# Kernel tuning notes

Measured on AMD Instinct MI355X. Metric: run time of the kernel, lower is better.

The kernel has to match this reference:

```python
import jax, jax.numpy as jnp
import numpy as np

E = 8          # num_experts
K = 2          # top-k experts per token
CAP_RATIO = 1.05


def setup_inputs() -> dict:
    key = jax.random.key(0)
    k0, k1, k2, k3 = jax.random.split(key, 4)
    B, S, D, H = 2, 2048, 512, 2048
    return {
        "x": jax.random.normal(k0, (B, S, D), jnp.float32),
        "gate_w": jax.random.normal(k1, (E, D), jnp.float32) * (1.0 / np.sqrt(D)),
        "fc1_w": jax.random.normal(k2, (E, D, H), jnp.float32) * (1.0 / np.sqrt(D)),
        "fc1_b": jnp.zeros((E, H), jnp.float32),
        "fc2_w": jax.random.normal(k3, (E, H, D), jnp.float32) * (1.0 / np.sqrt(H)),
        "fc2_b": jnp.zeros((E, D), jnp.float32),
    }


def reference(x, gate_w, fc1_w, fc1_b, fc2_w, fc2_b):
    B, S, D = x.shape
    xf = x.reshape(-1, D)               # [T, D]
    T = xf.shape[0]

    # ---- router (eval mode: no noise) ----
    logits = xf @ gate_w.T              # [T, E]
    gates = jax.nn.softmax(logits, axis=-1)
    top_g, top_i = jax.lax.top_k(gates, K)   # [T, K]

    # importance auxiliary loss (std unbiased=False == jnp.std default)
    imp = gates.sum(axis=0)                  # [E]
    imp_loss = (jnp.std(imp) / (imp.mean() + 1e-6)) ** 2

    # ---- capacity-limited dispatch mask ----
    # torch loops slot-major: slot 0 over all tokens in order, then slot 1.
    # position of each (slot, token) entry within its expert's queue:
    buffer_cap = round(K * T * CAP_RATIO / E)
    idx_sm = top_i.T.reshape(-1)                        # [K*T] slot-major
    oh = jax.nn.one_hot(idx_sm, E, dtype=jnp.int32)     # [K*T, E]
    pos = jnp.cumsum(oh, axis=0) - oh                   # earlier same-expert count
    pos_e = jnp.take_along_axis(pos, idx_sm[:, None], axis=1)[:, 0]
    within = (pos_e < buffer_cap).reshape(K, T).T       # [T, K] bool

    wf = within.astype(xf.dtype)
    oh_tke = jax.nn.one_hot(top_i, E, dtype=xf.dtype) * wf[..., None]  # dispatch mask [T,K,E]
    combine_te = jnp.einsum('tk,tke->te', top_g * wf, oh_tke / jnp.maximum(oh_tke, 1e-30) * oh_tke) if False else jnp.einsum('tk,tke->te', top_g * wf, jax.nn.one_hot(top_i, E, dtype=xf.dtype))

    # load-balance loss from post-capacity token counts
    tokens_per_expert = oh_tke.sum(axis=(0, 1))         # [E]
    l_load = (jnp.std(tokens_per_expert) / (tokens_per_expert.mean() + 1e-6)) ** 2
    l_aux = 0.5 * (imp_loss + l_load)

    # ---- per-expert MLP (dense compute, masked combine) ----
    h = jnp.einsum('td,edh->teh', xf, fc1_w) + fc1_b[None]      # [T, E, H]
    h = jax.nn.gelu(h, approximate=False)                       # torch nn.GELU default
    y = jnp.einsum('teh,ehd->ted', h, fc2_w) + fc2_b[None]      # [T, E, D]

    out = jnp.einsum('te,ted->td', combine_te, y).reshape(B, S, D)
    return out, l_aux, l_load
```

## Files before the change

### kernel.cpp

```cpp
#include <hip/hip_runtime.h>
#include <hip/hip_bf16.h>

#define E_    8
#define TT    4096
#define DD    512
#define HH    2048
#define CAP   1075
#define MPAD  1152
#define MT    9
#define MT2   18

typedef __bf16 bf16_t;
typedef bf16_t bf16x4 __attribute__((ext_vector_type(4)));
typedef bf16_t bf16x8 __attribute__((ext_vector_type(8)));
typedef float  f32x4  __attribute__((ext_vector_type(4)));
typedef unsigned int u32;

__device__ __forceinline__ bf16_t tobf(float f) { return (bf16_t)f; }

__device__ __forceinline__ float gelu_f(float v) {
  const float u = v * (0.7978845608028654f + 0.035677408136300125f * v * v);
  const float a = __builtin_fabsf(u);
  const float ex = __expf(2.0f * a);
  float th = 1.0f - 2.0f / (ex + 1.0f);
  th = __builtin_copysignf(th, u);
  return 0.5f * v * (1.0f + th);
}

#define OFF_TOPI  256u
#define OFF_TOPG  (OFF_TOPI + 4096u*2u*4u)
#define OFF_SLOT  (OFF_TOPG + 4096u*2u*4u)
#define OFF_ETOK  (OFF_SLOT + 4096u*2u*4u)
#define OFF_XB    (OFF_ETOK + 8u*1152u*4u)
#define XB_BYTES  (4096u*512u*2u)
#define OFF_W1T   (OFF_XB + XB_BYTES)
#define W1T_BYTES (8u*512u*2048u*2u)
#define OFF_W2T   (OFF_W1T + W1T_BYTES)
#define W2T_BYTES (8u*2048u*512u*2u)
#define OFF_H     (OFF_W2T + W2T_BYTES)
#define H_BYTES   (8u*1152u*2048u*2u)
#define OFF_Y     OFF_W1T

__global__ __launch_bounds__(256) void router_kernel(
    const float* __restrict__ x, const float* __restrict__ gw,
    float* __restrict__ imp, int* __restrict__ top_i, float* __restrict__ top_g,
    bf16_t* __restrict__ xb) {
  const int tid = threadIdx.x;
  const int wid = tid >> 6, lane = tid & 63;
  const int t = blockIdx.x * 4 + wid;

  float p[E_];
#pragma unroll
  for (int e = 0; e < E_; ++e) p[e] = 0.f;
  const float* xr = x + (size_t)t * DD;
  bf16_t* xo = xb + (size_t)t * DD;
#pragma unroll
  for (int it = 0; it < 2; ++it) {
    const int d = it * 256 + lane * 4;
    const float4 xv = *(const float4*)(xr + d);
    bf16_t o4[4] = {tobf(xv.x), tobf(xv.y), tobf(xv.z), tobf(xv.w)};
    *(bf16x4*)(xo + d) = *(const bf16x4*)o4;
#pragma unroll
    for (int e = 0; e < E_; ++e) {
      const float4 gv = *(const float4*)(gw + e * DD + d);
      p[e] += xv.x * gv.x + xv.y * gv.y + xv.z * gv.z + xv.w * gv.w;
    }
  }
#pragma unroll
  for (int off = 32; off > 0; off >>= 1) {
#pragma unroll
    for (int e = 0; e < E_; ++e) p[e] += __shfl_down(p[e], off);
  }

  __shared__ float simp[4][E_];
  if (lane == 0) {
    float mx = p[0];
#pragma unroll
    for (int e = 1; e < E_; ++e) mx = fmaxf(mx, p[e]);
    float g[E_]; float s = 0.f;
#pragma unroll
    for (int e = 0; e < E_; ++e) { g[e] = expf(p[e] - mx); s += g[e]; }
    const float inv = 1.f / s;
#pragma unroll
    for (int e = 0; e < E_; ++e) { g[e] *= inv; simp[wid][e] = g[e]; }
    int i0 = 0;
#pragma unroll
    for (int e = 1; e < E_; ++e) if (g[e] > g[i0]) i0 = e;
    int i1 = (i0 == 0) ? 1 : 0;
#pragma unroll
    for (int e = 0; e < E_; ++e) if (e != i0 && g[e] > g[i1]) i1 = e;
    top_i[t * 2 + 0] = i0;  top_i[t * 2 + 1] = i1;
    top_g[t * 2 + 0] = g[i0]; top_g[t * 2 + 1] = g[i1];
  }
  __syncthreads();
  if (tid < E_) {
    const float s = simp[0][tid] + simp[1][tid] + simp[2][tid] + simp[3][tid];
    atomicAdd(&imp[tid], s);
  }
}

__global__ __launch_bounds__(1024) void capacity_kernel(
    const int* __restrict__ top_i, const float* __restrict__ top_g,
    const float* __restrict__ imp, int* __restrict__ etok,
    int* __restrict__ slot_map, int* __restrict__ kept, float* __restrict__ scal) {
  __shared__ u32 wt[16][4];
  const int tid = threadIdx.x, wave = tid >> 6, lane = tid & 63;

  int eidx[8];
#pragma unroll
  for (int q = 0; q < 8; ++q) {
    const int j = tid * 8 + q;
    const int k = j >> 12, t = j & (TT - 1);
    eidx[q] = top_i[t * 2 + k];
  }
  u32 pk[4] = {0u, 0u, 0u, 0u};
#pragma unroll
  for (int q = 0; q < 8; ++q) pk[eidx[q] >> 1] += 1u << ((eidx[q] & 1) * 16);

  u32 v[4] = {pk[0], pk[1], pk[2], pk[3]};
#pragma unroll
  for (int off = 1; off < 64; off <<= 1) {
#pragma unroll
    for (int p = 0; p < 4; ++p) {
      const u32 n = (u32)__shfl_up((int)v[p], off);
      if (lane >= off) v[p] += n;
    }
  }
  if (lane == 63) {
#pragma unroll
    for (int p = 0; p < 4; ++p) wt[wave][p] = v[p];
  }
  __syncthreads();
  u32 base[4] = {0u, 0u, 0u, 0u}, tot[4] = {0u, 0u, 0u, 0u};
#pragma unroll
  for (int w = 0; w < 16; ++w) {
#pragma unroll
    for (int p = 0; p < 4; ++p) {
      const u32 xv = wt[w][p];
      if (w < wave) base[p] += xv;
      tot[p] += xv;
    }
  }
  int run[E_];
#pragma unroll
  for (int p = 0; p < 4; ++p) {
    const u32 excl = base[p] + v[p] - pk[p];
    run[2 * p]     = (int)(excl & 0xFFFFu);
    run[2 * p + 1] = (int)(excl >> 16);
  }
#pragma unroll
  for (int q = 0; q < 8; ++q) {
    const int e = eidx[q];
    const int pos = run[e]++;
    const int j = tid * 8 + q;
    if (pos < CAP) {
      const int k = j >> 12, t = j & (TT - 1);
      etok[e * MPAD + pos] = t;
      slot_map[j] = (e << 16) | pos;
    } else {
      slot_map[j] = -1;
    }
  }
  if (tid == 0) {
    float tpe[E_];
#pragma unroll
    for (int p = 0; p < 4; ++p) {
      const int t0 = (int)(tot[p] & 0xFFFFu), t1 = (int)(tot[p] >> 16);
      const int k0 = t0 < CAP ? t0 : CAP, k1 = t1 < CAP ? t1 : CAP;
      kept[2 * p] = k0; kept[2 * p + 1] = k1;
      tpe[2 * p] = (float)k0; tpe[2 * p + 1] = (float)k1;
    }
    float ms = 0.f;
#pragma unroll
    for (int e = 0; e < E_; ++e) ms += tpe[e];
    ms *= (1.f / E_);
    float vt = 0.f;
#pragma unroll
    for (int e = 0; e < E_; ++e) { const float d = tpe[e] - ms; vt += d * d; }
    vt *= (1.f / E_);
    const float ll = vt / ((ms + 1e-6f) * (ms + 1e-6f));

    float iv[E_], mi = 0.f;
#pragma unroll
    for (int e = 0; e < E_; ++e) { iv[e] = imp[e]; mi += iv[e]; }
    mi *= (1.f / E_);
    float vi = 0.f;
#pragma unroll
    for (int e = 0; e < E_; ++e) { const float d = iv[e] - mi; vi += d * d; }
    vi *= (1.f / E_);
    const float il = vi / ((mi + 1e-6f) * (mi + 1e-6f));

    scal[0] = 0.5f * (il + ll);
    scal[1] = ll;
  }
}

__global__ __launch_bounds__(256) void transpose_both_kernel(
    const float* __restrict__ fc1, bf16_t* __restrict__ w1t,
    const float* __restrict__ fc2, bf16_t* __restrict__ w2t) {
  __shared__ float tile[64][65];
  const int z = blockIdx.z;
  const bool first = (z < 8);
  const int e = first ? z : z - 8;
  const int R = first ? DD : HH;
  const int C = first ? HH : DD;
  const int ct = first ? blockIdx.x : blockIdx.y;
  const int rt = first ? blockIdx.y : blockIdx.x;
  const float* ip = (first ? fc1 : fc2) + (size_t)e * DD * HH;
  bf16_t* op = (first ? w1t : w2t) + (size_t)e * DD * HH;
  const int r0 = rt * 64, c0 = ct * 64;
  const int tid = threadIdx.x;
  const int rr = tid >> 4, c4 = (tid & 15) * 4;
#pragma unroll
  for (int p = 0; p < 4; ++p) {
    const int r = p * 16 + rr;
    const float4 v = *(const float4*)(ip + (size_t)(r0 + r) * C + c0 + c4);
    tile[r][c4 + 0] = v.x; tile[r][c4 + 1] = v.y;
    tile[r][c4 + 2] = v.z; tile[r][c4 + 3] = v.w;
  }
  __syncthreads();
  const int g = tid & 7, ob = tid >> 3;
#pragma unroll
  for (int p = 0; p < 2; ++p) {
    const int oc = p * 32 + ob;
    bf16_t o8[8];
#pragma unroll
    for (int k = 0; k < 8; ++k) o8[k] = tobf(tile[g * 8 + k][oc]);
    *(bf16x8*)(op + (size_t)(c0 + oc) * R + r0 + g * 8) = *(const bf16x8*)o8;
  }
}

template <int MI, int KLEN, int KSTR, bool GATHER>
__device__ __forceinline__ void gemm_core(
    const bf16_t* __restrict__ Abase, const int* __restrict__ rows,
    const bf16_t* __restrict__ B,
    bf16_t* As, bf16_t* Bs, f32x4 (&acc)[4][MI]) {
  const int tid = threadIdx.x;
  const int wave = tid >> 6, lane = tid & 63;
  const int r8 = lane >> 3;
  const int kswz = ((lane & 7) ^ r8) * 8;
  const bf16_t* ga[MI];
#pragma unroll
  for (int p = 0; p < MI; ++p) {
    const int r = wave * (MI * 8) + p * 8 + r8;
    const int trow = GATHER ? rows[r] : r;
    ga[p] = Abase + (size_t)trow * KSTR + kswz;
  }
  const bf16_t* gb = B + (size_t)(wave * 32 + r8) * KSTR + kswz;
  const int mw = (wave >> 1) * (MI * 16), nw = (wave & 1) * 64;
  const int l15 = lane & 15, quad = lane >> 4;
  const int sw = l15 & 7;

  for (int k0 = 0; k0 < KLEN; k0 += 64) {
    __syncthreads();
#pragma unroll
    for (int p = 0; p < MI; ++p) {
      __builtin_amdgcn_global_load_lds(
          (const __attribute__((address_space(1))) void*)(ga[p] + k0),
          (__attribute__((address_space(3))) void*)(As + (wave * (MI * 8) + p * 8) * 64),
          16, 0, 0);
    }
#pragma unroll
    for (int p = 0; p < 4; ++p) {
      __builtin_amdgcn_global_load_lds(
          (const __attribute__((address_space(1))) void*)(gb + (size_t)p * 8 * KSTR + k0),
          (__attribute__((address_space(3))) void*)(Bs + (wave * 32 + p * 8) * 64),
          16, 0, 0);
    }
    __syncthreads();
#pragma unroll
    for (int ks = 0; ks < 2; ++ks) {
      bf16x8 af[MI], bfr[4];
#pragma unroll
      for (int i = 0; i < MI; ++i)
        af[i] = *(const bf16x8*)(As + (mw + i * 16 + l15) * 64 + (((ks * 4 + quad) ^ sw) << 3));
#pragma unroll
      for (int j = 0; j < 4; ++j)
        bfr[j] = *(const bf16x8*)(Bs + (nw + j * 16 + l15) * 64 + (((ks * 4 + quad) ^ sw) << 3));
#pragma unroll
      for (int j = 0; j < 4; ++j)
#pragma unroll
        for (int i = 0; i < MI; ++i)
          acc[j][i] = __builtin_amdgcn_mfma_f32_16x16x32_bf16(bfr[j], af[i], acc[j][i], 0, 0, 0);
    }
  }
}

__global__ __launch_bounds__(256, 4) void gemm1_kernel(
    const bf16_t* __restrict__ xb, const int* __restrict__ etok,
    const int* __restrict__ kept, const bf16_t* __restrict__ W1t,
    const float* __restrict__ b1, bf16_t* __restrict__ Hbuf) {
  const int e = blockIdx.x, tileN = blockIdx.y, tileM = blockIdx.z;
  if (tileM * 128 >= kept[e]) return;
  __shared__ __align__(16) bf16_t As[128 * 64];
  __shared__ __align__(16) bf16_t Bs[128 * 64];
  const bf16_t* B = W1t + ((size_t)e * HH + tileN * 128) * DD;
  f32x4 acc[4][4];
  const f32x4 z = {0.f, 0.f, 0.f, 0.f};
#pragma unroll
  for (int j = 0; j < 4; ++j)
#pragma unroll
    for (int i = 0; i < 4; ++i) acc[j][i] = z;
  gemm_core<4, DD, DD, true>(xb, etok + e * MPAD + tileM * 128, B, As, Bs, acc);

  const int tid = threadIdx.x, wave = tid >> 6, lane = tid & 63;
  const int mw = (wave >> 1) * 64, nw = (wave & 1) * 64;
  const int l15 = lane & 15, quad = lane >> 4;
#pragma unroll
  for (int j = 0; j < 4; ++j) {
    const int n0 = tileN * 128 + nw + j * 16 + quad * 4;
    const float4 b4 = *(const float4*)(b1 + e * HH + n0);
#pragma unroll
    for (int i = 0; i < 4; ++i) {
      const int m = tileM * 128 + mw + i * 16 + l15;
      bf16x4 h4;
      h4.x = tobf(gelu_f(acc[j][i][0] + b4.x));
      h4.y = tobf(gelu_f(acc[j][i][1] + b4.y));
      h4.z = tobf(gelu_f(acc[j][i][2] + b4.z));
      h4.w = tobf(gelu_f(acc[j][i][3] + b4.w));
      *(bf16x4*)(Hbuf + ((size_t)e * MPAD + m) * HH + n0) = h4;
    }
  }
}

__global__ __launch_bounds__(256, 6) void gemm2_kernel(
    const bf16_t* __restrict__ Hbuf, const bf16_t* __restrict__ W2t,
    const int* __restrict__ kept, bf16_t* __restrict__ Ybuf) {
  const int e = blockIdx.x, tileN = blockIdx.y, tileM = blockIdx.z;
  const int nk = kept[e];
  if (tileM * 64 >= nk) return;
  __shared__ __align__(16) bf16_t As[64 * 64];
  __shared__ __align__(16) bf16_t Bs[128 * 64];
  const bf16_t* A = Hbuf + ((size_t)e * MPAD + tileM * 64) * HH;
  const bf16_t* B = W2t + ((size_t)e * DD + tileN * 128) * HH;
  f32x4 acc[4][2];
  const f32x4 z = {0.f, 0.f, 0.f, 0.f};
#pragma unroll
  for (int j = 0; j < 4; ++j)
#pragma unroll
    for (int i = 0; i < 2; ++i) acc[j][i] = z;
  gemm_core<2, HH, HH, false>(A, nullptr, B, As, Bs, acc);

  const int tid = threadIdx.x, wave = tid >> 6, lane = tid & 63;
  const int mw = (wave >> 1) * 32, nw = (wave & 1) * 64;
  const int l15 = lane & 15, quad = lane >> 4;
#pragma unroll
  for (int j = 0; j < 4; ++j) {
    const int n0 = tileN * 128 + nw + j * 16 + quad * 4;
#pragma unroll
    for (int i = 0; i < 2; ++i) {
      const int m = tileM * 64 + mw + i * 16 + l15;
      if (m < nk) {
        bf16x4 o4;
        o4.x = tobf(acc[j][i][0]);
        o4.y = tobf(acc[j][i][1]);
        o4.z = tobf(acc[j][i][2]);
        o4.w = tobf(acc[j][i][3]);
        *(bf16x4*)(Ybuf + ((size_t)e * MPAD + m) * DD + n0) = o4;
      }
    }
  }
}

__global__ __launch_bounds__(128) void combine_kernel(
    const bf16_t* __restrict__ Ybuf, const float* __restrict__ b2,
    const int* __restrict__ slot_map, const float* __restrict__ top_g,
    float* __restrict__ out) {
  const int t = blockIdx.x;
  const int c = threadIdx.x * 4;
  float4 acc = {0.f, 0.f, 0.f, 0.f};
#pragma unroll
  for (int k = 0; k < 2; ++k) {
    const int sm = slot_map[k * TT + t];
    if (sm >= 0) {
      const int e = sm >> 16, pos = sm & 0xFFFF;
      const float w = top_g[t * 2 + k];
      const bf16x4 y4 = *(const bf16x4*)(Ybuf + ((size_t)e * MPAD + pos) * DD + c);
      const float4 bb = *(const float4*)(b2 + e * DD + c);
      acc.x += w * ((float)y4.x + bb.x);
      acc.y += w * ((float)y4.y + bb.y);
      acc.z += w * ((float)y4.z + bb.z);
      acc.w += w * ((float)y4.w + bb.w);
    }
  }
  *(float4*)(out + (size_t)t * DD + c) = acc;
}

extern "C" void kernel_launch(void* const* d_in, const int* in_sizes, int n_in,
                              void* d_out, int out_size, void* d_ws, size_t ws_size,
                              hipStream_t stream) {
  const float* x      = (const float*)d_in[0];
  const float* gate_w = (const float*)d_in[1];
  const float* fc1_w  = (const float*)d_in[2];
  const float* fc1_b  = (const float*)d_in[3];
  const float* fc2_w  = (const float*)d_in[4];
  const float* fc2_b  = (const float*)d_in[5];
  float* out = (float*)d_out;

  char* ws = (char*)d_ws;
  float*  imp   = (float*)(ws + 0);
  int*    kept  = (int*)(ws + 64);
  int*    top_i = (int*)(ws + OFF_TOPI);
  float*  top_g = (float*)(ws + OFF_TOPG);
  int*    slotm = (int*)(ws + OFF_SLOT);
  int*    etok  = (int*)(ws + OFF_ETOK);
  bf16_t* xb    = (bf16_t*)(ws + OFF_XB);
  bf16_t* W1t   = (bf16_t*)(ws + OFF_W1T);
  bf16_t* W2t   = (bf16_t*)(ws + OFF_W2T);
  bf16_t* Hbuf  = (bf16_t*)(ws + OFF_H);
  bf16_t* Ybuf  = (bf16_t*)(ws + OFF_Y);
  float*  scal  = out + (size_t)TT * DD;

  hipMemsetAsync(ws, 0, 256, stream);
  hipMemsetAsync(ws + OFF_ETOK, 0, E_ * MPAD * 4, stream);

  transpose_both_kernel<<<dim3(32, 8, 16), 256, 0, stream>>>(fc1_w, W1t, fc2_w, W2t);

  router_kernel<<<TT / 4, 256, 0, stream>>>(x, gate_w, imp, top_i, top_g, xb);
  capacity_kernel<<<1, 1024, 0, stream>>>(top_i, top_g, imp, etok, slotm, kept, scal);

  gemm1_kernel<<<dim3(E_, HH / 128, MT), 256, 0, stream>>>(xb, etok, kept, W1t, fc1_b, Hbuf);
  gemm2_kernel<<<dim3(E_, DD / 128, MT2), 256, 0, stream>>>(Hbuf, W2t, kept, Ybuf);
  combine_kernel<<<TT, 128, 0, stream>>>(Ybuf, fc2_b, slotm, top_g, out);
}
```

Baseline: 220.0 us.

## Double-buffer LDS tiles in MoE GEMMs and merge workspace memsets

Splits the GEMM core's K loop into a two-stage ping-pong that issues global-to-LDS loads for the next K step while MFMAs run on the current buffer, which cuts the number of barriers per step from two to one. Doubling shared memory per block lowers the occupancy hints (4→2 for gemm1, 6→3 for gemm2). It also moves the etok array next to the header so that a single memset clears both, removing one memset call. The risk is that lower occupancy hides less latency than the added software pipelining gains.

Measured after the change: 225.2 us. 1.02x slower.

```diff
diff --git a/kernel.cpp b/kernel.cpp
--- a/kernel.cpp
+++ b/kernel.cpp
@@ -27,11 +27,11 @@
   return 0.5f * v * (1.0f + th);
 }
 
-#define OFF_TOPI  256u
+#define OFF_ETOK  256u
+#define OFF_TOPI  (OFF_ETOK + 8u*1152u*4u)
 #define OFF_TOPG  (OFF_TOPI + 4096u*2u*4u)
 #define OFF_SLOT  (OFF_TOPG + 4096u*2u*4u)
-#define OFF_ETOK  (OFF_SLOT + 4096u*2u*4u)
-#define OFF_XB    (OFF_ETOK + 8u*1152u*4u)
+#define OFF_XB    (OFF_SLOT + 4096u*2u*4u)
 #define XB_BYTES  (4096u*512u*2u)
 #define OFF_W1T   (OFF_XB + XB_BYTES)
 #define W1T_BYTES (8u*512u*2048u*2u)
@@ -235,6 +235,8 @@
     const bf16_t* __restrict__ Abase, const int* __restrict__ rows,
     const bf16_t* __restrict__ B,
     bf16_t* As, bf16_t* Bs, f32x4 (&acc)[4][MI]) {
+  constexpr int ASZ = MI * 32 * 64;
+  constexpr int BSZ = 128 * 64;
   const int tid = threadIdx.x;
   const int wave = tid >> 6, lane = tid & 63;
   const int r8 = lane >> 3;
@@ -251,49 +253,67 @@
   const int l15 = lane & 15, quad = lane >> 4;
   const int sw = l15 & 7;
 
-  for (int k0 = 0; k0 < KLEN; k0 += 64) {
-    __syncthreads();
-#pragma unroll
-    for (int p = 0; p < MI; ++p) {
+  auto stage = [&](int k0, int buf) {
+    bf16_t* as = As + buf * ASZ + (wave * (MI * 8)) * 64;
+    bf16_t* bs = Bs + buf * BSZ + (wave * 32) * 64;
+#pragma unroll
+    for (int p = 0; p < MI; ++p)
       __builtin_amdgcn_global_load_lds(
           (const __attribute__((address_space(1))) void*)(ga[p] + k0),
-          (__attribute__((address_space(3))) void*)(As + (wave * (MI * 8) + p * 8) * 64),
-          16, 0, 0);
-    }
-#pragma unroll
-    for (int p = 0; p < 4; ++p) {
+          (__attribute__((address_space(3))) void*)(as + p * 8 * 64), 16, 0, 0);
+#pragma unroll
+    for (int p = 0; p < 4; ++p)
       __builtin_amdgcn_global_load_lds(
           (const __attribute__((address_space(1))) void*)(gb + (size_t)p * 8 * KSTR + k0),
-          (__attribute__((address_space(3))) void*)(Bs + (wave * 32 + p * 8) * 64),
-          16, 0, 0);
-    }
-    __syncthreads();
+          (__attribute__((address_space(3))) void*)(bs + p * 8 * 64), 16, 0, 0);
+  };
+  auto compute = [&](int buf) {
+    const bf16_t* as = As + buf * ASZ;
+    const bf16_t* bs = Bs + buf * BSZ;
 #pragma unroll
     for (int ks = 0; ks < 2; ++ks) {
       bf16x8 af[MI], bfr[4];
 #pragma unroll
       for (int i = 0; i < MI; ++i)
-        af[i] = *(const bf16x8*)(As + (mw + i * 16 + l15) * 64 + (((ks * 4 + quad) ^ sw) << 3));
+        af[i] = *(const bf16x8*)(as + (mw + i * 16 + l15) * 64 + (((ks * 4 + quad) ^ sw) << 3));
 #pragma unroll
       for (int j = 0; j < 4; ++j)
-        bfr[j] = *(const bf16x8*)(Bs + (nw + j * 16 + l15) * 64 + (((ks * 4 + quad) ^ sw) << 3));
+        bfr[j] = *(const bf16x8*)(bs + (nw + j * 16 + l15) * 64 + (((ks * 4 + quad) ^ sw) << 3));
 #pragma unroll
       for (int j = 0; j < 4; ++j)
 #pragma unroll
         for (int i = 0; i < MI; ++i)
           acc[j][i] = __builtin_amdgcn_mfma_f32_16x16x32_bf16(bfr[j], af[i], acc[j][i], 0, 0, 0);
     }
-  }
-}
-
-__global__ __launch_bounds__(256, 4) void gemm1_kernel(
+  };
+
+  static_assert((KLEN / 64) % 2 == 0, "even K-step count");
+  constexpr int NS = KLEN / 64;
+  stage(0, 0);
+  __syncthreads();
+#pragma unroll
+  for (int sp = 0; sp < NS / 2 - 1; ++sp) {
+    stage((2 * sp + 1) * 64, 1);
+    compute(0);
+    __syncthreads();
+    stage((2 * sp + 2) * 64, 0);
+    compute(1);
+    __syncthreads();
+  }
+  stage((NS - 1) * 64, 1);
+  compute(0);
+  __syncthreads();
+  compute(1);
+}
+
+__global__ __launch_bounds__(256, 2) void gemm1_kernel(
     const bf16_t* __restrict__ xb, const int* __restrict__ etok,
     const int* __restrict__ kept, const bf16_t* __restrict__ W1t,
     const float* __restrict__ b1, bf16_t* __restrict__ Hbuf) {
   const int e = blockIdx.x, tileN = blockIdx.y, tileM = blockIdx.z;
   if (tileM * 128 >= kept[e]) return;
-  __shared__ __align__(16) bf16_t As[128 * 64];
-  __shared__ __align__(16) bf16_t Bs[128 * 64];
+  __shared__ __align__(16) bf16_t As[2 * 128 * 64];
+  __shared__ __align__(16) bf16_t Bs[2 * 128 * 64];
   const bf16_t* B = W1t + ((size_t)e * HH + tileN * 128) * DD;
   f32x4 acc[4][4];
   const f32x4 z = {0.f, 0.f, 0.f, 0.f};
@@ -323,14 +343,14 @@
   }
 }
 
-__global__ __launch_bounds__(256, 6) void gemm2_kernel(
+__global__ __launch_bounds__(256, 3) void gemm2_kernel(
     const bf16_t* __restrict__ Hbuf, const bf16_t* __restrict__ W2t,
     const int* __restrict__ kept, bf16_t* __restrict__ Ybuf) {
   const int e = blockIdx.x, tileN = blockIdx.y, tileM = blockIdx.z;
   const int nk = kept[e];
   if (tileM * 64 >= nk) return;
-  __shared__ __align__(16) bf16_t As[64 * 64];
-  __shared__ __align__(16) bf16_t Bs[128 * 64];
+  __shared__ __align__(16) bf16_t As[2 * 64 * 64];
+  __shared__ __align__(16) bf16_t Bs[2 * 128 * 64];
   const bf16_t* A = Hbuf + ((size_t)e * MPAD + tileM * 64) * HH;
   const bf16_t* B = W2t + ((size_t)e * DD + tileN * 128) * HH;
   f32x4 acc[4][2];
@@ -400,10 +420,10 @@
   char* ws = (char*)d_ws;
   float*  imp   = (float*)(ws + 0);
   int*    kept  = (int*)(ws + 64);
+  int*    etok  = (int*)(ws + OFF_ETOK);
   int*    top_i = (int*)(ws + OFF_TOPI);
   float*  top_g = (float*)(ws + OFF_TOPG);
   int*    slotm = (int*)(ws + OFF_SLOT);
-  int*    etok  = (int*)(ws + OFF_ETOK);
   bf16_t* xb    = (bf16_t*)(ws + OFF_XB);
   bf16_t* W1t   = (bf16_t*)(ws + OFF_W1T);
   bf16_t* W2t   = (bf16_t*)(ws + OFF_W2T);
@@ -411,8 +431,7 @@
   bf16_t* Ybuf  = (bf16_t*)(ws + OFF_Y);
   float*  scal  = out + (size_t)TT * DD;
 
-  hipMemsetAsync(ws, 0, 256, stream);
-  hipMemsetAsync(ws + OFF_ETOK, 0, E_ * MPAD * 4, stream);
+  hipMemsetAsync(ws, 0, OFF_TOPI, stream);
 
   transpose_both_kernel<<<dim3(32, 8, 16), 256, 0, stream>>>(fc1_w, W1t, fc2_w, W2t);
 
```

## Generalize GEMM core tiling; widen gemm1 N tile, deepen gemm2 K step, merge memsets

Applied to the files above, without the earlier changes.

The GEMM core is templated on wave count, tile rows/cols and K sub-steps. gemm1 now runs 512-thread blocks over 128x256 tiles, so each gathered A tile is reused across twice as many output columns. gemm2 loads two 64-wide K slices per barrier pair, halving the synchronizations over its long K loop at the cost of twice the LDS and lower occupancy (launch bound lowered from 6 to 4). The etok buffer is moved next to the header so a single memset clears both, removing one memset call.

Measured after the change: 219.8 us. No clear change (-0.1%).

```diff
diff --git a/kernel.cpp b/kernel.cpp
--- a/kernel.cpp
+++ b/kernel.cpp
@@ -27,11 +27,11 @@
   return 0.5f * v * (1.0f + th);
 }
 
-#define OFF_TOPI  256u
+#define OFF_ETOK  256u
+#define OFF_TOPI  (OFF_ETOK + 8u*1152u*4u)
 #define OFF_TOPG  (OFF_TOPI + 4096u*2u*4u)
 #define OFF_SLOT  (OFF_TOPG + 4096u*2u*4u)
-#define OFF_ETOK  (OFF_SLOT + 4096u*2u*4u)
-#define OFF_XB    (OFF_ETOK + 8u*1152u*4u)
+#define OFF_XB    (OFF_SLOT + 4096u*2u*4u)
 #define XB_BYTES  (4096u*512u*2u)
 #define OFF_W1T   (OFF_XB + XB_BYTES)
 #define W1T_BYTES (8u*512u*2048u*2u)
@@ -230,53 +230,60 @@
   }
 }
 
-template <int MI, int KLEN, int KSTR, bool GATHER>
+template <int NW, int MR, int NC, int MI, int KSUB, int KLEN, int KSTR, bool GATHER>
 __device__ __forceinline__ void gemm_core(
     const bf16_t* __restrict__ Abase, const int* __restrict__ rows,
     const bf16_t* __restrict__ B,
     bf16_t* As, bf16_t* Bs, f32x4 (&acc)[4][MI]) {
+  constexpr int NWC = NC / 64;
+  constexpr int AIW = MR / (8 * NW);
+  constexpr int BIW = NC / (8 * NW);
   const int tid = threadIdx.x;
   const int wave = tid >> 6, lane = tid & 63;
   const int r8 = lane >> 3;
   const int kswz = ((lane & 7) ^ r8) * 8;
-  const bf16_t* ga[MI];
-#pragma unroll
-  for (int p = 0; p < MI; ++p) {
-    const int r = wave * (MI * 8) + p * 8 + r8;
+  const bf16_t* ga[AIW];
+#pragma unroll
+  for (int p = 0; p < AIW; ++p) {
+    const int r = (wave * AIW + p) * 8 + r8;
     const int trow = GATHER ? rows[r] : r;
     ga[p] = Abase + (size_t)trow * KSTR + kswz;
   }
-  const bf16_t* gb = B + (size_t)(wave * 32 + r8) * KSTR + kswz;
-  const int mw = (wave >> 1) * (MI * 16), nw = (wave & 1) * 64;
+  const bf16_t* gb = B + (size_t)(wave * BIW * 8 + r8) * KSTR + kswz;
+  const int mw = (wave / NWC) * (MI * 16), nw = (wave % NWC) * 64;
   const int l15 = lane & 15, quad = lane >> 4;
   const int sw = l15 & 7;
 
-  for (int k0 = 0; k0 < KLEN; k0 += 64) {
+  for (int kb = 0; kb < KLEN; kb += KSUB * 64) {
     __syncthreads();
 #pragma unroll
-    for (int p = 0; p < MI; ++p) {
-      __builtin_amdgcn_global_load_lds(
-          (const __attribute__((address_space(1))) void*)(ga[p] + k0),
-          (__attribute__((address_space(3))) void*)(As + (wave * (MI * 8) + p * 8) * 64),
-          16, 0, 0);
-    }
-#pragma unroll
-    for (int p = 0; p < 4; ++p) {
-      __builtin_amdgcn_global_load_lds(
-          (const __attribute__((address_space(1))) void*)(gb + (size_t)p * 8 * KSTR + k0),
-          (__attribute__((address_space(3))) void*)(Bs + (wave * 32 + p * 8) * 64),
-          16, 0, 0);
+    for (int ks = 0; ks < KSUB; ++ks) {
+      const int k0 = kb + ks * 64;
+#pragma unroll
+      for (int p = 0; p < AIW; ++p)
+        __builtin_amdgcn_global_load_lds(
+            (const __attribute__((address_space(1))) void*)(ga[p] + k0),
+            (__attribute__((address_space(3))) void*)(As + (ks * MR + (wave * AIW + p) * 8) * 64),
+            16, 0, 0);
+#pragma unroll
+      for (int p = 0; p < BIW; ++p)
+        __builtin_amdgcn_global_load_lds(
+            (const __attribute__((address_space(1))) void*)(gb + (size_t)p * 8 * KSTR + k0),
+            (__attribute__((address_space(3))) void*)(Bs + (ks * NC + (wave * BIW + p) * 8) * 64),
+            16, 0, 0);
     }
     __syncthreads();
 #pragma unroll
-    for (int ks = 0; ks < 2; ++ks) {
+    for (int kh = 0; kh < KSUB * 2; ++kh) {
+      const int kt = kh >> 1;
+      const int kc = (((kh & 1) * 4 + quad) ^ sw) << 3;
       bf16x8 af[MI], bfr[4];
 #pragma unroll
       for (int i = 0; i < MI; ++i)
-        af[i] = *(const bf16x8*)(As + (mw + i * 16 + l15) * 64 + (((ks * 4 + quad) ^ sw) << 3));
+        af[i] = *(const bf16x8*)(As + (kt * MR + mw + i * 16 + l15) * 64 + kc);
 #pragma unroll
       for (int j = 0; j < 4; ++j)
-        bfr[j] = *(const bf16x8*)(Bs + (nw + j * 16 + l15) * 64 + (((ks * 4 + quad) ^ sw) << 3));
+        bfr[j] = *(const bf16x8*)(Bs + (kt * NC + nw + j * 16 + l15) * 64 + kc);
 #pragma unroll
       for (int j = 0; j < 4; ++j)
 #pragma unroll
@@ -286,29 +293,29 @@
   }
 }
 
-__global__ __launch_bounds__(256, 4) void gemm1_kernel(
+__global__ __launch_bounds__(512, 4) void gemm1_kernel(
     const bf16_t* __restrict__ xb, const int* __restrict__ etok,
     const int* __restrict__ kept, const bf16_t* __restrict__ W1t,
     const float* __restrict__ b1, bf16_t* __restrict__ Hbuf) {
   const int e = blockIdx.x, tileN = blockIdx.y, tileM = blockIdx.z;
   if (tileM * 128 >= kept[e]) return;
   __shared__ __align__(16) bf16_t As[128 * 64];
-  __shared__ __align__(16) bf16_t Bs[128 * 64];
-  const bf16_t* B = W1t + ((size_t)e * HH + tileN * 128) * DD;
+  __shared__ __align__(16) bf16_t Bs[256 * 64];
+  const bf16_t* B = W1t + ((size_t)e * HH + tileN * 256) * DD;
   f32x4 acc[4][4];
   const f32x4 z = {0.f, 0.f, 0.f, 0.f};
 #pragma unroll
   for (int j = 0; j < 4; ++j)
 #pragma unroll
     for (int i = 0; i < 4; ++i) acc[j][i] = z;
-  gemm_core<4, DD, DD, true>(xb, etok + e * MPAD + tileM * 128, B, As, Bs, acc);
+  gemm_core<8, 128, 256, 4, 1, DD, DD, true>(xb, etok + e * MPAD + tileM * 128, B, As, Bs, acc);
 
   const int tid = threadIdx.x, wave = tid >> 6, lane = tid & 63;
-  const int mw = (wave >> 1) * 64, nw = (wave & 1) * 64;
+  const int mw = (wave >> 2) * 64, nw = (wave & 3) * 64;
   const int l15 = lane & 15, quad = lane >> 4;
 #pragma unroll
   for (int j = 0; j < 4; ++j) {
-    const int n0 = tileN * 128 + nw + j * 16 + quad * 4;
+    const int n0 = tileN * 256 + nw + j * 16 + quad * 4;
     const float4 b4 = *(const float4*)(b1 + e * HH + n0);
 #pragma unroll
     for (int i = 0; i < 4; ++i) {
@@ -323,14 +330,14 @@
   }
 }
 
-__global__ __launch_bounds__(256, 6) void gemm2_kernel(
+__global__ __launch_bounds__(256, 4) void gemm2_kernel(
     const bf16_t* __restrict__ Hbuf, const bf16_t* __restrict__ W2t,
     const int* __restrict__ kept, bf16_t* __restrict__ Ybuf) {
   const int e = blockIdx.x, tileN = blockIdx.y, tileM = blockIdx.z;
   const int nk = kept[e];
   if (tileM * 64 >= nk) return;
-  __shared__ __align__(16) bf16_t As[64 * 64];
-  __shared__ __align__(16) bf16_t Bs[128 * 64];
+  __shared__ __align__(16) bf16_t As[2 * 64 * 64];
+  __shared__ __align__(16) bf16_t Bs[2 * 128 * 64];
   const bf16_t* A = Hbuf + ((size_t)e * MPAD + tileM * 64) * HH;
   const bf16_t* B = W2t + ((size_t)e * DD + tileN * 128) * HH;
   f32x4 acc[4][2];
@@ -339,7 +346,7 @@
   for (int j = 0; j < 4; ++j)
 #pragma unroll
     for (int i = 0; i < 2; ++i) acc[j][i] = z;
-  gemm_core<2, HH, HH, false>(A, nullptr, B, As, Bs, acc);
+  gemm_core<4, 64, 128, 2, 2, HH, HH, false>(A, nullptr, B, As, Bs, acc);
 
   const int tid = threadIdx.x, wave = tid >> 6, lane = tid & 63;
   const int mw = (wave >> 1) * 32, nw = (wave & 1) * 64;
@@ -400,10 +407,10 @@
   char* ws = (char*)d_ws;
   float*  imp   = (float*)(ws + 0);
   int*    kept  = (int*)(ws + 64);
+  int*    etok  = (int*)(ws + OFF_ETOK);
   int*    top_i = (int*)(ws + OFF_TOPI);
   float*  top_g = (float*)(ws + OFF_TOPG);
   int*    slotm = (int*)(ws + OFF_SLOT);
-  int*    etok  = (int*)(ws + OFF_ETOK);
   bf16_t* xb    = (bf16_t*)(ws + OFF_XB);
   bf16_t* W1t   = (bf16_t*)(ws + OFF_W1T);
   bf16_t* W2t   = (bf16_t*)(ws + OFF_W2T);
@@ -411,15 +418,14 @@
   bf16_t* Ybuf  = (bf16_t*)(ws + OFF_Y);
   float*  scal  = out + (size_t)TT * DD;
 
-  hipMemsetAsync(ws, 0, 256, stream);
-  hipMemsetAsync(ws + OFF_ETOK, 0, E_ * MPAD * 4, stream);
+  hipMemsetAsync(ws, 0, OFF_TOPI, stream);
 
   transpose_both_kernel<<<dim3(32, 8, 16), 256, 0, stream>>>(fc1_w, W1t, fc2_w, W2t);
 
   router_kernel<<<TT / 4, 256, 0, stream>>>(x, gate_w, imp, top_i, top_g, xb);
   capacity_kernel<<<1, 1024, 0, stream>>>(top_i, top_g, imp, etok, slotm, kept, scal);
 
-  gemm1_kernel<<<dim3(E_, HH / 128, MT), 256, 0, stream>>>(xb, etok, kept, W1t, fc1_b, Hbuf);
+  gemm1_kernel<<<dim3(E_, HH / 256, MT), 512, 0, stream>>>(xb, etok, kept, W1t, fc1_b, Hbuf);
   gemm2_kernel<<<dim3(E_, DD / 128, MT2), 256, 0, stream>>>(Hbuf, W2t, kept, Ybuf);
   combine_kernel<<<TT, 128, 0, stream>>>(Ybuf, fc2_b, slotm, top_g, out);
 }
```
